# Kernel optimization log

Measured on AMD Instinct MI355X. Metric: run time of the kernel, lower is better.

The kernel has to match this reference:

```python
import jax, jax.numpy as jnp
import numpy as np

N = 2048          # batch
T = 50            # max_num_visit
CODES = 40        # codes per visit
VOCAB = 527       # max_tokens for CategoryEncoding
MH = VOCAB - 1    # 526 after dropping column 0
AUX = 10          # aux_info feature dim
E = 256           # config.embedding_dim (LSTM units)


def setup_inputs() -> dict:
    key = jax.random.key(0)
    ks = jax.random.split(key, 10)
    code = jax.random.randint(ks[0], (N, T, CODES), 0, VOCAB, dtype=jnp.int32)
    aux_info = jax.random.normal(ks[1], (N, T, AUX), jnp.float32)
    length = jax.random.randint(ks[2], (N,), 1, T + 1, dtype=jnp.int32)

    def glorot(k, shape):
        fan = shape[0]
        return jax.random.normal(k, shape, jnp.float32) * (1.0 / np.sqrt(fan))

    W_lin = glorot(ks[3], (MH + AUX, E)); b_lin = jnp.zeros((E,), jnp.float32)
    K_lstm = glorot(ks[4], (E, 4 * E))
    R_lstm = glorot(ks[5], (E, 4 * E))
    b_lstm = jnp.zeros((4 * E,), jnp.float32)
    W0 = glorot(ks[6], (E, 256)); b0 = jnp.zeros((256,), jnp.float32)
    W1 = glorot(ks[7], (256, 256)); b1 = jnp.zeros((256,), jnp.float32)
    return dict(code=code, aux_info=aux_info, length=length, is_training=0,
                W_lin=W_lin, b_lin=b_lin, K_lstm=K_lstm, R_lstm=R_lstm,
                b_lstm=b_lstm, W0=W0, b0=b0, W1=W1, b1=b1)


def _multi_hot(code):
    # CategoryEncoding binary mode: presence indicator over vocab, drop col 0
    flat = code.reshape(N * T, CODES)
    mh = jnp.zeros((N * T, VOCAB), jnp.float32)
    mh = mh.at[jnp.arange(N * T)[:, None], flat].set(1.0)
    return mh[:, 1:].reshape(N, T, MH)


def _lstm(x, K, R, b):
    # Keras LSTM, gate order [i, f, g(c), o]; inference (dropout off)
    xz = jnp.einsum('nte,eh->nth', x, K) + b          # [N,T,4E]
    xz = jnp.transpose(xz, (1, 0, 2))                  # [T,N,4E]

    def step(carry, zt):
        h, c = carry
        z = zt + h @ R
        i, f, g, o = jnp.split(z, 4, axis=-1)
        c = jax.nn.sigmoid(f) * c + jax.nn.sigmoid(i) * jnp.tanh(g)
        h = jax.nn.sigmoid(o) * jnp.tanh(c)
        return (h, c), h

    h0 = jnp.zeros((N, E), jnp.float32)
    (_, _), hs = jax.lax.scan(step, (h0, h0), xz)
    return jnp.transpose(hs, (1, 0, 2))                # [N,T,E]


def reference(code, aux_info, length, is_training,
              W_lin, b_lin, K_lstm, R_lstm, b_lstm, W0, b0, W1, b1):
    mh = _multi_hot(code)                              # [N,T,526]
    x = jax.nn.relu(jnp.concatenate([mh, aux_info], axis=-1) @ W_lin + b_lin)
    h = _lstm(x, K_lstm, R_lstm, b_lstm)               # [N,T,E]
    x_last = h[jnp.arange(N), length - 1]              # gather_nd: last valid step
    fv = jax.nn.relu(x_last @ W0 + b0) @ W1 + b1
    fv = fv / jnp.sqrt(jnp.sum(fv ** 2, axis=-1, keepdims=True))
    return fv
```

## Files before the change

kernel.cpp:

```cpp
#include <hip/hip_runtime.h>
#include <hip/hip_bf16.h>
#include <math.h>
#include <stdint.h>

#define N_BATCH 2048
#define T_STEPS 50
#define NCODES  40
#define MH      526
#define AUXD    10
#define WLROWS  536
#define E_DIM   256
#define G_DIM   1024
#define TCHUNK  10
#define MBLK    64
#define NFUSED  (TCHUNK * 32)

typedef __attribute__((ext_vector_type(8))) short short8;
typedef __attribute__((ext_vector_type(4))) short short4v;
typedef __attribute__((ext_vector_type(4))) float f32x4;
typedef __attribute__((ext_vector_type(4))) int   i32x4;

__device__ __forceinline__ short f2bf(float f) {
    __hip_bfloat16 h = __float2bfloat16(f);
    return *reinterpret_cast<short*>(&h);
}
__device__ __forceinline__ float bf2f(unsigned short u) {
    return __uint_as_float(((unsigned int)u) << 16);
}
__device__ __forceinline__ float sigf(float x) {
    return 1.f / (1.f + __expf(-x));
}
__device__ __forceinline__ float tanhfast(float x) {
    return 2.f / (1.f + __expf(-2.f * x)) - 1.f;
}

__global__ __launch_bounds__(256) void k_zero(int* __restrict__ cnt)
{
    const int i = blockIdx.x * 256 + threadIdx.x;
    if (i < 3 * 64 * 32) cnt[i] = 0;
}

__global__ __launch_bounds__(256) void k_prep_wcoop(
    const float* __restrict__ R, short* __restrict__ Wcoop)
{
    const int gid  = blockIdx.x * 256 + threadIdx.x;
    const int fg   = gid >> 6, lane = gid & 63;
    const int p    = lane >> 4, lr = lane & 15;
    const int kk   = fg & 7;
    const int g    = (fg >> 3) & 3;
    const int w    = (fg >> 5) & 3;
    const int cs   = fg >> 7;
    const int n    = g * 256 + cs * 64 + w * 16 + lr;
    short* dst = Wcoop + (size_t)fg * 512 + lane * 8;
    #pragma unroll
    for (int j = 0; j < 8; ++j)
        dst[j] = f2bf(R[(size_t)(kk * 32 + p * 8 + j) * G_DIM + n]);
}

__global__ __launch_bounds__(256) void k_prep_wfk(
    const float* __restrict__ K, short* __restrict__ WfK)
{
    const int gid  = blockIdx.x * 256 + threadIdx.x;
    const int fg   = gid >> 6, lane = gid & 63;
    const int p    = lane >> 4, lr = lane & 15;
    const int kb   = fg >> 6;
    const int cb   = (fg >> 3) & 7;
    const int w    = fg & 7;
    const int n    = w * 128 + cb * 16 + lr;
    short* dst = WfK + (size_t)fg * 512 + lane * 8;
    #pragma unroll
    for (int j = 0; j < 8; ++j)
        dst[j] = f2bf(K[(size_t)(kb * 32 + p * 8 + j) * G_DIM + n]);
}

__global__ __launch_bounds__(256) void k_prep_wfl(
    const float* __restrict__ W_lin, short* __restrict__ WfL)
{
    const int gid  = blockIdx.x * 256 + threadIdx.x;
    const int fg   = gid >> 6, lane = gid & 63;
    const int p    = lane >> 4, lr = lane & 15;
    const int kk   = fg >> 4;
    const int cb   = (fg >> 3) & 1;
    const int w    = fg & 7;
    const int n    = w * 32 + cb * 16 + lr;
    short* dst = WfL + (size_t)fg * 512 + lane * 8;
    #pragma unroll
    for (int j = 0; j < 8; ++j) {
        const int k = kk * 32 + p * 8 + j;
        dst[j] = (k < WLROWS) ? f2bf(W_lin[(size_t)k * E_DIM + n]) : (short)0;
    }
}

__global__ __launch_bounds__(512, 1) void k_fused(
    const int* __restrict__ code, const float* __restrict__ aux,
    const short* __restrict__ WfL, const float* __restrict__ b_lin,
    const short* __restrict__ WfK, short* __restrict__ xzp, int t0f)
{
    const int tid  = threadIdx.x;
    const int w    = tid >> 6;
    const int lane = tid & 63;
    const int lr   = lane & 15;
    const int p    = lane >> 4;
    const int fid  = blockIdx.x;
    const int tl   = fid >> 5;
    const int ngg  = fid & 31;
    const int n0   = ngg * MBLK;
    const int t    = t0f + tl;
    const int ph8  = (fid >> 3) & 7;
    const int ph17 = (fid >> 3) % 17;

    __shared__ __align__(16) short oh[MBLK][552];
    __shared__ __align__(16) short xs[MBLK][264];

    for (int i = tid; i < (MBLK * 552) / 8; i += 512)
        ((int4*)&oh[0][0])[i] = (int4){0, 0, 0, 0};
    __syncthreads();

    for (int i = tid; i < MBLK * NCODES; i += 512) {
        const int r = i / NCODES;
        const int j = i - r * NCODES;
        const int c = code[((size_t)(n0 + r) * T_STEPS + t) * NCODES + j];
        if (c > 0) ((unsigned short*)&oh[0][0])[r * 552 + (c - 1)] = 0x3F80;
    }
    for (int i = tid; i < MBLK * AUXD; i += 512) {
        const int r = i / AUXD;
        const int a = i - r * AUXD;
        oh[r][MH + a] = f2bf(aux[((size_t)(n0 + r) * T_STEPS + t) * AUXD + a]);
    }
    __syncthreads();

    const short* wfl_thr = WfL + (size_t)w * 512 + lane * 8;
    const short* wfk_thr = WfK + (size_t)w * 512 + lane * 8;

    {
        f32x4 acc[4][2];
        #pragma unroll
        for (int rb = 0; rb < 4; ++rb)
            #pragma unroll
            for (int cb = 0; cb < 2; ++cb)
                acc[rb][cb] = (f32x4){0.f, 0.f, 0.f, 0.f};

        for (int kk = 0; kk < 17; ++kk) {
            int kx = kk + ph17; if (kx >= 17) kx -= 17;
            short8 a[4];
            #pragma unroll
            for (int rb = 0; rb < 4; ++rb)
                a[rb] = *(const short8*)&oh[rb * 16 + lr][kx * 32 + p * 8];
            #pragma unroll
            for (int cb = 0; cb < 2; ++cb) {
                short8 bf = *(const short8*)(wfl_thr + (size_t)(kx * 2 + cb) * 4096);
                #pragma unroll
                for (int rb = 0; rb < 4; ++rb)
                    acc[rb][cb] = __builtin_amdgcn_mfma_f32_16x16x32_bf16(
                        a[rb], bf, acc[rb][cb], 0, 0, 0);
            }
        }
        float bias[2];
        #pragma unroll
        for (int cb = 0; cb < 2; ++cb) bias[cb] = b_lin[w * 32 + cb * 16 + lr];
        #pragma unroll
        for (int rb = 0; rb < 4; ++rb)
            #pragma unroll
            for (int cb = 0; cb < 2; ++cb)
                #pragma unroll
                for (int rr = 0; rr < 4; ++rr)
                    xs[rb * 16 + p * 4 + rr][w * 32 + cb * 16 + lr] =
                        f2bf(fmaxf(acc[rb][cb][rr] + bias[cb], 0.f));
        __syncthreads();
    }

    #pragma unroll
    for (int half = 0; half < 2; ++half) {
        f32x4 acc[4][4];
        #pragma unroll
        for (int rb = 0; rb < 4; ++rb)
            #pragma unroll
            for (int c4 = 0; c4 < 4; ++c4)
                acc[rb][c4] = (f32x4){0.f, 0.f, 0.f, 0.f};

        for (int kb = 0; kb < 8; ++kb) {
            const int kx = (kb + ph8) & 7;
            short8 a[4];
            #pragma unroll
            for (int rb = 0; rb < 4; ++rb)
                a[rb] = *(const short8*)&xs[rb * 16 + lr][kx * 32 + p * 8];
            #pragma unroll
            for (int c4 = 0; c4 < 4; ++c4) {
                const int cb = half * 4 + c4;
                short8 bf = *(const short8*)(wfk_thr + (size_t)(kx * 8 + cb) * 4096);
                #pragma unroll
                for (int rb = 0; rb < 4; ++rb)
                    acc[rb][c4] = __builtin_amdgcn_mfma_f32_16x16x32_bf16(
                        a[rb], bf, acc[rb][c4], 0, 0, 0);
            }
        }
        #pragma unroll
        for (int rb = 0; rb < 4; ++rb) {
            const int rgg = ngg * 4 + rb;
            #pragma unroll
            for (int c4 = 0; c4 < 4; ++c4) {
                const int cb = half * 4 + c4;
                const int c0 = w * 128 + cb * 16;
                const int g  = c0 >> 8;
                const int wp = (c0 >> 5) & 7;
                const int eb = (c0 >> 4) & 1;
                const int j8 = eb * 4 + g;
                short4v v;
                #pragma unroll
                for (int rr = 0; rr < 4; ++rr) v[rr] = f2bf(acc[rb][c4][rr]);
                *(short4v*)(xzp +
                    (((size_t)rgg * TCHUNK + tl) * 64 + wp * 8 + j8) * 256 +
                    lane * 4) = v;
            }
        }
    }
}

__global__ __launch_bounds__(256, 1) void k_rcoop(
    const short* __restrict__ xz0, const short* __restrict__ xz1,
    const int* __restrict__ length,
    const short* __restrict__ Wcoop, const float* __restrict__ b,
    short* __restrict__ h_buf, float* __restrict__ c_state,
    float* __restrict__ xlast, int* __restrict__ flags,
    int t0, int nsteps)
{
    const int tid  = threadIdx.x;
    const int w    = tid >> 6;
    const int lane = tid & 63;
    const int lr   = lane & 15;
    const int p    = lane >> 4;
    const int cs   = blockIdx.x >> 6;
    const int rg   = blockIdx.x & 63;
    const int r0   = rg * 32;
    const int e    = cs * 64 + w * 16 + lr;

    __shared__ __align__(16) short h_f[2][8][512];
    __shared__ __align__(16) short h_o[32][64];
    __shared__ int s_len[32];
    if (tid < 32) s_len[tid] = length[r0 + tid];

    short8 bw[4][8];
    {
        const short* wb = Wcoop + ((size_t)((cs * 4 + w) * 4)) * 8 * 512 + lane * 8;
        #pragma unroll
        for (int g = 0; g < 4; ++g)
            #pragma unroll
            for (int kk = 0; kk < 8; ++kk)
                bw[g][kk] = *(const short8*)(wb + (size_t)(g * 8 + kk) * 512);
    }

    float bias[4];
    #pragma unroll
    for (int g = 0; g < 4; ++g) bias[g] = b[g * 256 + e];

    float creg[2][4];
    if (t0 == 0) {
        #pragma unroll
        for (int rf = 0; rf < 2; ++rf)
            #pragma unroll
            for (int rr = 0; rr < 4; ++rr) creg[rf][rr] = 0.f;
    } else {
        #pragma unroll
        for (int rf = 0; rf < 2; ++rf)
            #pragma unroll
            for (int rr = 0; rr < 4; ++rr)
                creg[rf][rr] = c_state[(size_t)(r0 + rf * 16 + p * 4 + rr) * E_DIM + e];
    }
    __syncthreads();

    int len_r[2][4];
    #pragma unroll
    for (int rf = 0; rf < 2; ++rf)
        #pragma unroll
        for (int rr = 0; rr < 4; ++rr)
            len_r[rf][rr] = s_len[rf * 16 + p * 4 + rr];

    const uint64_t slot_addr = (uint64_t)(uintptr_t)(flags + rg * 32 + cs);
    const uint64_t line_addr = (uint64_t)(uintptr_t)(flags + rg * 32);
    int bcnt = 0;

#define PEERS_BARRIER()                                                        \
    do {                                                                       \
        ++bcnt;                                                                \
        __syncthreads();               \
        if (tid == 0) {                                                        \
            asm volatile("global_store_dword %0, %1, off sc0 sc1"              \
                         :: "v"(slot_addr), "v"(bcnt) : "memory");             \
            i32x4 fv;                                                          \
            do {                                                               \
                asm volatile("global_load_dwordx4 %0, %1, off sc0 sc1\n\t"     \
                             "s_waitcnt vmcnt(0)"                              \
                             : "=v"(fv) : "v"(line_addr) : "memory");          \
            } while (fv[0] < bcnt || fv[1] < bcnt ||                           \
                     fv[2] < bcnt || fv[3] < bcnt);                            \
        }                                                                      \
        __syncthreads();                                                       \
    } while (0)

    if (t0 == 0) {
        const i32x4 z4 = {0, 0, 0, 0};
        const int row = tid >> 3, seg = tid & 7;
        const uint64_t dst = (uint64_t)(uintptr_t)(h_buf +
            (size_t)(r0 + row) * E_DIM + cs * 64 + seg * 8);
        asm volatile("global_store_dwordx4 %0, %1, off sc0 sc1"
                     :: "v"(dst), "v"(z4) : "memory");
        PEERS_BARRIER();
    }

    const short* hb0 = h_buf;
    const short* hb1 = h_buf + (size_t)N_BATCH * E_DIM;
    const size_t coloff = (size_t)((cs * 2 + (w >> 1)) * 8 + (w & 1) * 4) * 256 +
                          lane * 4;
    const size_t rowoff0 = (size_t)(2 * rg + 0) * TCHUNK * 16384;
    const size_t rowoff1 = (size_t)(2 * rg + 1) * TCHUNK * 16384;

#define XZ_BASE(T, RFOFF)                                                      \
    ((((((T) / TCHUNK) & 1) ? xz1 : xz0)) + (RFOFF) +                          \
     (size_t)((T) % TCHUNK) * 16384 + coloff)

    short4v xv[2][4];
    {
        const short* b0p = XZ_BASE(t0, rowoff0);
        const short* b1p = XZ_BASE(t0, rowoff1);
        #pragma unroll
        for (int g = 0; g < 4; ++g) {
            xv[0][g] = *(const short4v*)(b0p + g * 256);
            xv[1][g] = *(const short4v*)(b1p + g * 256);
        }
    }

    const int ld_row = tid >> 5;
    const int ld_ch  = tid & 31;
    const int ld_kk  = ld_ch >> 2;

    for (int s = 0; s < nsteps; ++s) {
        const int t = t0 + s;
        const short* hb_r = (t & 1) ? hb1 : hb0;

        {
            short8 ld[4];
            #pragma unroll
            for (int it = 0; it < 4; ++it) {
                const int row = ld_row + it * 8;
                const uint64_t src = (uint64_t)(uintptr_t)(hb_r +
                    (size_t)(r0 + row) * E_DIM + ld_ch * 8);
                asm volatile("global_load_dwordx4 %0, %1, off sc0 sc1"
                             : "=&v"(ld[it]) : "v"(src) : "memory");
            }
            asm volatile("s_waitcnt vmcnt(0)" ::: "memory");
            #pragma unroll
            for (int it = 0; it < 4; ++it) {
                const int row  = ld_row + it * 8;
                const int slot = (((ld_ch & 3) * 16) + (row & 15)) ^ ld_kk;
                *(short8*)&h_f[row >> 4][ld_kk][slot * 8] = ld[it];
            }
        }
        __syncthreads();

        f32x4 acc[2][4];
        #pragma unroll
        for (int rf = 0; rf < 2; ++rf)
            #pragma unroll
            for (int g = 0; g < 4; ++g)
                #pragma unroll
                for (int rr = 0; rr < 4; ++rr)
                    acc[rf][g][rr] = bf2f((unsigned short)xv[rf][g][rr]);

        #pragma unroll
        for (int kk = 0; kk < 8; ++kk) {
            const int sl = (lane ^ kk) * 8;
            short8 a0 = *(const short8*)&h_f[0][kk][sl];
            short8 a1 = *(const short8*)&h_f[1][kk][sl];
            #pragma unroll
            for (int g = 0; g < 4; ++g) {
                acc[0][g] = __builtin_amdgcn_mfma_f32_16x16x32_bf16(
                    a0, bw[g][kk], acc[0][g], 0, 0, 0);
                acc[1][g] = __builtin_amdgcn_mfma_f32_16x16x32_bf16(
                    a1, bw[g][kk], acc[1][g], 0, 0, 0);
            }
        }

        if (s + 1 < nsteps) {
            const short* b0p = XZ_BASE(t + 1, rowoff0);
            const short* b1p = XZ_BASE(t + 1, rowoff1);
            #pragma unroll
            for (int g = 0; g < 4; ++g) {
                xv[0][g] = *(const short4v*)(b0p + g * 256);
                xv[1][g] = *(const short4v*)(b1p + g * 256);
            }
        }

        #pragma unroll
        for (int rf = 0; rf < 2; ++rf) {
            #pragma unroll
            for (int rr = 0; rr < 4; ++rr) {
                float zi = acc[rf][0][rr] + bias[0];
                float zf = acc[rf][1][rr] + bias[1];
                float zg = acc[rf][2][rr] + bias[2];
                float zo = acc[rf][3][rr] + bias[3];
                float ig = sigf(zi), fg = sigf(zf);
                float gg = tanhfast(zg), og = sigf(zo);
                float cc = fg * creg[rf][rr] + ig * gg;
                float hh = og * tanhfast(cc);
                creg[rf][rr] = cc;
                h_o[rf * 16 + p * 4 + rr][w * 16 + lr] = f2bf(hh);
                const int row = r0 + rf * 16 + p * 4 + rr;
                if (t == len_r[rf][rr] - 1)
                    xlast[(size_t)row * E_DIM + e] = hh;
            }
        }
        __syncthreads();

        {
            short* hb_w = (short*)(((t + 1) & 1) ? hb1 : hb0);
            const int row = tid >> 3, seg = tid & 7;
            i32x4 v = *(const i32x4*)&h_o[row][seg * 8];
            const uint64_t dst = (uint64_t)(uintptr_t)(hb_w +
                (size_t)(r0 + row) * E_DIM + cs * 64 + seg * 8);
            asm volatile("global_store_dwordx4 %0, %1, off sc0 sc1"
                         :: "v"(dst), "v"(v) : "memory");
        }

        if (s + 1 < nsteps) PEERS_BARRIER();
    }

    #pragma unroll
    for (int rf = 0; rf < 2; ++rf)
        #pragma unroll
        for (int rr = 0; rr < 4; ++rr)
            c_state[(size_t)(r0 + rf * 16 + p * 4 + rr) * E_DIM + e] = creg[rf][rr];
#undef PEERS_BARRIER
#undef XZ_BASE
}

__global__ __launch_bounds__(256) void k_head(
    const float* __restrict__ xlast,
    const float* __restrict__ W0, const float* __restrict__ b0,
    const float* __restrict__ W1, const float* __restrict__ b1,
    float* __restrict__ out)
{
    const int n = blockIdx.x;
    const int j = threadIdx.x;

    __shared__ __align__(16) float xsh[E_DIM];
    __shared__ __align__(16) float y0[E_DIM];
    __shared__ float part[4];

    xsh[j] = xlast[(size_t)n * E_DIM + j];
    __syncthreads();

    float acc = b0[j];
    for (int k4 = 0; k4 < E_DIM; k4 += 4) {
        float4 xv = *reinterpret_cast<const float4*>(&xsh[k4]);
        #pragma unroll
        for (int kk = 0; kk < 4; ++kk)
            acc += (&xv.x)[kk] * W0[(size_t)(k4 + kk) * E_DIM + j];
    }
    y0[j] = fmaxf(acc, 0.f);
    __syncthreads();

    acc = b1[j];
    for (int k4 = 0; k4 < E_DIM; k4 += 4) {
        float4 yv = *reinterpret_cast<const float4*>(&y0[k4]);
        #pragma unroll
        for (int kk = 0; kk < 4; ++kk)
            acc += (&yv.x)[kk] * W1[(size_t)(k4 + kk) * E_DIM + j];
    }

    float sq = acc * acc;
    #pragma unroll
    for (int off = 32; off > 0; off >>= 1)
        sq += __shfl_xor(sq, off, 64);
    if ((j & 63) == 0) part[j >> 6] = sq;
    __syncthreads();
    float total = part[0] + part[1] + part[2] + part[3];

    out[(size_t)n * E_DIM + j] = acc * rsqrtf(total);
}

extern "C" void kernel_launch(void* const* d_in, const int* in_sizes, int n_in,
                              void* d_out, int out_size, void* d_ws, size_t ws_size,
                              hipStream_t stream) {
    const int*   code   = (const int*)  d_in[0];
    const float* aux    = (const float*)d_in[1];
    const int*   length = (const int*)  d_in[2];
    const float* W_lin  = (const float*)d_in[4];
    const float* b_lin  = (const float*)d_in[5];
    const float* K      = (const float*)d_in[6];
    const float* R      = (const float*)d_in[7];
    const float* b      = (const float*)d_in[8];
    const float* W0     = (const float*)d_in[9];
    const float* b0     = (const float*)d_in[10];
    const float* W1     = (const float*)d_in[11];
    const float* b1     = (const float*)d_in[12];
    float* out = (float*)d_out;

    char* ws = (char*)d_ws;
    short* Wcoop   = (short*)(ws + 0);
    short* WfK     = (short*)(ws + 524288);
    short* WfL     = (short*)(ws + 1048576);
    float* xlast   = (float*)(ws + 1327104);
    float* c_state = (float*)(ws + 3424256);
    short* h_buf   = (short*)(ws + 5521408);
    int*   flags   = (int*)  (ws + 7618560);
    short* xzp0    = (short*)(ws + 7643136);
    short* xzp1    = (short*)(ws + 49586176);

    k_zero      <<<24,  256, 0, stream>>>(flags);
    k_prep_wcoop<<<128, 256, 0, stream>>>(R, Wcoop);
    k_prep_wfk  <<<128, 256, 0, stream>>>(K, WfK);
    k_prep_wfl  <<<68,  256, 0, stream>>>(W_lin, WfL);

    k_fused<<<NFUSED, 512, 0, stream>>>(code, aux, WfL, b_lin, WfK, xzp0, 0);
    k_fused<<<NFUSED, 512, 0, stream>>>(code, aux, WfL, b_lin, WfK, xzp1, 10);
    k_rcoop<<<256, 256, 0, stream>>>(xzp0, xzp1, length, Wcoop, b, h_buf,
                                     c_state, xlast, flags + 0 * 2048, 0, 20);
    k_fused<<<NFUSED, 512, 0, stream>>>(code, aux, WfL, b_lin, WfK, xzp0, 20);
    k_fused<<<NFUSED, 512, 0, stream>>>(code, aux, WfL, b_lin, WfK, xzp1, 30);
    k_rcoop<<<256, 256, 0, stream>>>(xzp0, xzp1, length, Wcoop, b, h_buf,
                                     c_state, xlast, flags + 1 * 2048, 20, 20);
    k_fused<<<NFUSED, 512, 0, stream>>>(code, aux, WfL, b_lin, WfK, xzp0, 40);
    k_rcoop<<<256, 256, 0, stream>>>(xzp0, xzp1, length, Wcoop, b, h_buf,
                                     c_state, xlast, flags + 2 * 2048, 40, 10);

    k_head<<<N_BATCH, 256, 0, stream>>>(xlast, W0, b0, W1, b1, out);
}
```

Before: 425.1 us.

## Double fused-kernel row tile to 128 and split multi-hot K into two halves

```diff
diff --git a/kernel.cpp b/kernel.cpp
--- a/kernel.cpp
+++ b/kernel.cpp
@@ -12,8 +12,8 @@
 #define E_DIM   256
 #define G_DIM   1024
 #define TCHUNK  10
-#define MBLK    64
-#define NFUSED  (TCHUNK * 32)
+#define FROWS   128
+#define NFUSED  (TCHUNK * 16)
 
 typedef __attribute__((ext_vector_type(8))) short short8;
 typedef __attribute__((ext_vector_type(4))) short short4v;
@@ -102,101 +102,110 @@
     const int lr   = lane & 15;
     const int p    = lane >> 4;
     const int fid  = blockIdx.x;
-    const int tl   = fid >> 5;
-    const int ngg  = fid & 31;
-    const int n0   = ngg * MBLK;
+    const int tl   = fid >> 4;
+    const int ngg  = fid & 15;
+    const int n0   = ngg * FROWS;
     const int t    = t0f + tl;
-    const int ph8  = (fid >> 3) & 7;
-    const int ph17 = (fid >> 3) % 17;
-
-    __shared__ __align__(16) short oh[MBLK][552];
-    __shared__ __align__(16) short xs[MBLK][264];
-
-    for (int i = tid; i < (MBLK * 552) / 8; i += 512)
-        ((int4*)&oh[0][0])[i] = (int4){0, 0, 0, 0};
-    __syncthreads();
-
-    for (int i = tid; i < MBLK * NCODES; i += 512) {
-        const int r = i / NCODES;
-        const int j = i - r * NCODES;
-        const int c = code[((size_t)(n0 + r) * T_STEPS + t) * NCODES + j];
-        if (c > 0) ((unsigned short*)&oh[0][0])[r * 552 + (c - 1)] = 0x3F80;
-    }
-    for (int i = tid; i < MBLK * AUXD; i += 512) {
-        const int r = i / AUXD;
-        const int a = i - r * AUXD;
-        oh[r][MH + a] = f2bf(aux[((size_t)(n0 + r) * T_STEPS + t) * AUXD + a]);
-    }
-    __syncthreads();
-
-    const short* wfl_thr = WfL + (size_t)w * 512 + lane * 8;
-    const short* wfk_thr = WfK + (size_t)w * 512 + lane * 8;
+
+    __shared__ __align__(16) short oh[FROWS][288];
+    __shared__ __align__(16) short xs[FROWS][264];
+
+    f32x4 acc2[8][2];
+    #pragma unroll
+    for (int rb = 0; rb < 8; ++rb)
+        #pragma unroll
+        for (int cb = 0; cb < 2; ++cb)
+            acc2[rb][cb] = (f32x4){0.f, 0.f, 0.f, 0.f};
+
+    for (int kh = 0; kh < 2; ++kh) {
+        const int c0  = kh ? 288 : 0;
+        const int Wd  = kh ? 256 : 288;
+        const int nk  = kh ? 8 : 9;
+        const int kk0 = kh ? 9 : 0;
+
+        for (int i = tid; i < (FROWS * 288) / 8; i += 512)
+            ((int4*)&oh[0][0])[i] = (int4){0, 0, 0, 0};
+        __syncthreads();
+
+        for (int i = tid; i < FROWS * NCODES; i += 512) {
+            const int r = i / NCODES;
+            const int j = i - r * NCODES;
+            const int c = code[((size_t)(n0 + r) * T_STEPS + t) * NCODES + j];
+            const int cm1 = c - 1;
+            if (c > 0 && cm1 >= c0 && cm1 < c0 + Wd)
+                oh[r][cm1 - c0] = 0x3F80;
+        }
+        if (kh == 1) {
+            for (int i = tid; i < FROWS * AUXD; i += 512) {
+                const int r = i / AUXD;
+                const int a = i - r * AUXD;
+                oh[r][MH - 288 + a] =
+                    f2bf(aux[((size_t)(n0 + r) * T_STEPS + t) * AUXD + a]);
+            }
+        }
+        __syncthreads();
+
+        for (int kx = 0; kx < nk; ++kx) {
+            short8 a[8];
+            #pragma unroll
+            for (int rb = 0; rb < 8; ++rb)
+                a[rb] = *(const short8*)&oh[rb * 16 + lr][kx * 32 + p * 8];
+            #pragma unroll
+            for (int cb = 0; cb < 2; ++cb) {
+                short8 bf = *(const short8*)(WfL +
+                    (size_t)(((kk0 + kx) * 2 + cb) * 8 + w) * 512 + lane * 8);
+                #pragma unroll
+                for (int rb = 0; rb < 8; ++rb)
+                    acc2[rb][cb] = __builtin_amdgcn_mfma_f32_16x16x32_bf16(
+                        a[rb], bf, acc2[rb][cb], 0, 0, 0);
+            }
+        }
+        __syncthreads();
+    }
 
     {
-        f32x4 acc[4][2];
-        #pragma unroll
-        for (int rb = 0; rb < 4; ++rb)
-            #pragma unroll
-            for (int cb = 0; cb < 2; ++cb)
-                acc[rb][cb] = (f32x4){0.f, 0.f, 0.f, 0.f};
-
-        for (int kk = 0; kk < 17; ++kk) {
-            int kx = kk + ph17; if (kx >= 17) kx -= 17;
-            short8 a[4];
-            #pragma unroll
-            for (int rb = 0; rb < 4; ++rb)
-                a[rb] = *(const short8*)&oh[rb * 16 + lr][kx * 32 + p * 8];
-            #pragma unroll
-            for (int cb = 0; cb < 2; ++cb) {
-                short8 bf = *(const short8*)(wfl_thr + (size_t)(kx * 2 + cb) * 4096);
-                #pragma unroll
-                for (int rb = 0; rb < 4; ++rb)
-                    acc[rb][cb] = __builtin_amdgcn_mfma_f32_16x16x32_bf16(
-                        a[rb], bf, acc[rb][cb], 0, 0, 0);
-            }
-        }
         float bias[2];
         #pragma unroll
         for (int cb = 0; cb < 2; ++cb) bias[cb] = b_lin[w * 32 + cb * 16 + lr];
         #pragma unroll
-        for (int rb = 0; rb < 4; ++rb)
+        for (int rb = 0; rb < 8; ++rb)
             #pragma unroll
             for (int cb = 0; cb < 2; ++cb)
                 #pragma unroll
                 for (int rr = 0; rr < 4; ++rr)
                     xs[rb * 16 + p * 4 + rr][w * 32 + cb * 16 + lr] =
-                        f2bf(fmaxf(acc[rb][cb][rr] + bias[cb], 0.f));
+                        f2bf(fmaxf(acc2[rb][cb][rr] + bias[cb], 0.f));
         __syncthreads();
     }
 
+    const short* wfk_thr = WfK + (size_t)w * 512 + lane * 8;
     #pragma unroll
     for (int half = 0; half < 2; ++half) {
-        f32x4 acc[4][4];
-        #pragma unroll
-        for (int rb = 0; rb < 4; ++rb)
+        f32x4 acc[8][4];
+        #pragma unroll
+        for (int rb = 0; rb < 8; ++rb)
             #pragma unroll
             for (int c4 = 0; c4 < 4; ++c4)
                 acc[rb][c4] = (f32x4){0.f, 0.f, 0.f, 0.f};
 
         for (int kb = 0; kb < 8; ++kb) {
-            const int kx = (kb + ph8) & 7;
-            short8 a[4];
-            #pragma unroll
-            for (int rb = 0; rb < 4; ++rb)
-                a[rb] = *(const short8*)&xs[rb * 16 + lr][kx * 32 + p * 8];
+            short8 a[8];
+            #pragma unroll
+            for (int rb = 0; rb < 8; ++rb)
+                a[rb] = *(const short8*)&xs[rb * 16 + lr][kb * 32 + p * 8];
             #pragma unroll
             for (int c4 = 0; c4 < 4; ++c4) {
                 const int cb = half * 4 + c4;
-                short8 bf = *(const short8*)(wfk_thr + (size_t)(kx * 8 + cb) * 4096);
+                short8 bf = *(const short8*)(wfk_thr + (size_t)(kb * 8 + cb) * 4096);
                 #pragma unroll
-                for (int rb = 0; rb < 4; ++rb)
+                for (int rb = 0; rb < 8; ++rb)
                     acc[rb][c4] = __builtin_amdgcn_mfma_f32_16x16x32_bf16(
                         a[rb], bf, acc[rb][c4], 0, 0, 0);
             }
         }
         #pragma unroll
-        for (int rb = 0; rb < 4; ++rb) {
-            const int rgg = ngg * 4 + rb;
+        for (int rb = 0; rb < 8; ++rb) {
+            const int rgg = ngg * 8 + rb;
             #pragma unroll
             for (int c4 = 0; c4 < 4; ++c4) {
                 const int cb = half * 4 + c4;
```

After: 452.4 us. 6.4% more time.
